# Optimization experiments

Measured on AMD Instinct MI355X. Metric: run time of the kernel, lower is better.

## Reference

```python
import jax, jax.numpy as jnp
import numpy as np

D_MODEL = 1024
N_HEADS = 16
D_Q = D_MODEL // N_HEADS
NEG = float(-2**32 + 1)


def setup_inputs() -> dict:
    key = jax.random.key(0)
    ks = jax.random.split(key, 8)
    B, L = 8, 1024
    q = jax.random.normal(ks[0], (B, L, D_MODEL), dtype=jnp.float32)
    k = jax.random.normal(ks[1], (B, L, D_MODEL), dtype=jnp.float32)
    # causal subsequent mask: 1 above the diagonal (positions to be masked)
    subseq_mask = jnp.broadcast_to(
        jnp.triu(jnp.ones((L, L), dtype=jnp.int32), k=1), (B, L, L))
    s = 1.0 / np.sqrt(D_MODEL)
    Wq = jax.random.normal(ks[2], (D_MODEL, D_MODEL), dtype=jnp.float32) * s
    Wk = jax.random.normal(ks[3], (D_MODEL, D_MODEL), dtype=jnp.float32) * s
    Wv = jax.random.normal(ks[4], (D_MODEL, D_MODEL), dtype=jnp.float32) * s
    bq = jax.random.normal(ks[5], (D_MODEL,), dtype=jnp.float32) * 0.01
    bk = jax.random.normal(ks[6], (D_MODEL,), dtype=jnp.float32) * 0.01
    bv = jax.random.normal(ks[7], (D_MODEL,), dtype=jnp.float32) * 0.01
    return {"q": q, "k": k, "subseq_mask": subseq_mask,
            "Wq": Wq, "bq": bq, "Wk": Wk, "bk": bk, "Wv": Wv, "bv": bv}


def reference(q, k, subseq_mask, Wq, bq, Wk, bk, Wv, bv):
    B, Lq, _ = q.shape
    Lk = k.shape[1]
    residual = q
    # projections; heads laid out as (H, B, L, d_q) matching torch permute(2,0,1,3)
    qp = (q @ Wq + bq).reshape(B, Lq, N_HEADS, D_Q).transpose(2, 0, 1, 3)
    kp = (k @ Wk + bk).reshape(B, Lk, N_HEADS, D_Q).transpose(2, 0, 1, 3)
    vp = (k @ Wv + bv).reshape(B, Lk, N_HEADS, D_Q).transpose(2, 0, 1, 3)
    # scaled scores: (H, B, Lq, Lk)
    scores = jnp.einsum('hbqd,hbkd->hbqk', qp, kp) / np.sqrt(D_Q)
    # key mask from PROJECTED k (faithful to source)
    key_masks = jnp.sign(jnp.abs(jnp.sum(kp, -1)))          # (H, B, Lk)
    scores = jnp.where(key_masks[:, :, None, :] == 0, NEG, scores)
    # subsequence (causal) mask, replicated over heads
    scores = jnp.where(subseq_mask[None, :, :, :] == 1, NEG, scores)
    attn = jax.nn.softmax(scores, axis=-1)
    # post-softmax query mask from PROJECTED q (faithful to source)
    query_masks = jnp.sign(jnp.abs(jnp.sum(qp, -1)))        # (H, B, Lq)
    attn = attn * query_masks[:, :, :, None]
    # dropout is identity in eval/reference mode
    out = jnp.einsum('hbqk,hbkd->hbqd', attn, vp)           # (H, B, Lq, d_q)
    out = out.transpose(1, 2, 0, 3).reshape(B, Lq, N_HEADS * D_Q)
    return out + residual
```

## Files before the change

kernel.cpp:

```cpp
#include <hip/hip_runtime.h>
#include <cstdint>
#include <cstddef>

#define DM 1024
#define NH 16
#define DQ 64
#define NB 8
#define LSEQ 1024

typedef __attribute__((ext_vector_type(8))) short short8;
typedef __attribute__((ext_vector_type(4))) float floatx4;

__device__ __forceinline__ unsigned short f2bf(float f) {
  union { float f; unsigned u; } v; v.f = f;
  unsigned r = v.u + 0x7FFFu + ((v.u >> 16) & 1u);
  return (unsigned short)(r >> 16);
}
__device__ __forceinline__ float bf2f(unsigned short u) {
  union { unsigned u; float f; } v; v.u = ((unsigned)u) << 16;
  return v.f;
}

__device__ __forceinline__ void async_load16(const void* g, void* l) {
  __builtin_amdgcn_global_load_lds(
      (const __attribute__((address_space(1))) unsigned int*)g,
      (__attribute__((address_space(3))) unsigned int*)l, 16, 0, 0);
}

__global__ void convert_qk(const float* __restrict__ q, const float* __restrict__ k,
                           unsigned short* __restrict__ qb, unsigned short* __restrict__ kb) {
  size_t i = ((size_t)blockIdx.x * 256 + threadIdx.x) * 4;
  float4 a = *(const float4*)&q[i];
  ushort4 r;
  r.x = f2bf(a.x); r.y = f2bf(a.y); r.z = f2bf(a.z); r.w = f2bf(a.w);
  *(ushort4*)&qb[i] = r;
  float4 b = *(const float4*)&k[i];
  ushort4 s;
  s.x = f2bf(b.x); s.y = f2bf(b.y); s.z = f2bf(b.z); s.w = f2bf(b.w);
  *(ushort4*)&kb[i] = s;
}

__global__ void transpose_w(const float* __restrict__ Wq, const float* __restrict__ Wk,
                            const float* __restrict__ Wv, unsigned short* __restrict__ Wt) {
  int z = blockIdx.z;
  const float* W = (z == 0) ? Wq : (z == 1) ? Wk : Wv;
  __shared__ float tile[32][33];
  int n0 = blockIdx.x * 32, k0 = blockIdx.y * 32;
  int tx = threadIdx.x;
  for (int j = threadIdx.y; j < 32; j += 8)
    tile[j][tx] = W[(size_t)(k0 + j) * DM + n0 + tx];
  __syncthreads();
  unsigned short* o = Wt + (size_t)z * DM * DM;
  for (int j = threadIdx.y; j < 32; j += 8)
    o[(size_t)(n0 + j) * DM + k0 + tx] = f2bf(tile[tx][j]);
}

__global__ __launch_bounds__(256) void gemm_proj(
    const unsigned short* __restrict__ qb, const unsigned short* __restrict__ kb,
    const unsigned short* __restrict__ Wt,
    const float* __restrict__ bq, const float* __restrict__ bk, const float* __restrict__ bv,
    unsigned short* __restrict__ Pq, unsigned short* __restrict__ Pk,
    unsigned short* __restrict__ Pvt,
    float* __restrict__ qmask, float* __restrict__ kmask) {
  const int z = blockIdx.z;
  const unsigned short* A = (z == 0) ? qb : kb;
  const unsigned short* Bt = Wt + (size_t)z * DM * DM;
  const float* bias = (z == 0) ? bq : (z == 1) ? bk : bv;

  __shared__ unsigned short smem[8704];
  unsigned short* As = smem;
  unsigned short* Bs = smem + 4096;

  const int tid = threadIdx.x;
  const int lane = tid & 63;
  const int wave = tid >> 6;
  const int l16 = lane & 15, quad = lane >> 4;
  const int wm = wave & 1, wn = wave >> 1;
  const int rowBase = blockIdx.y * 128;
  const int colBase = blockIdx.x * 128;

  floatx4 acc[4][4];
  const floatx4 zf = {0.f, 0.f, 0.f, 0.f};
#pragma unroll
  for (int i = 0; i < 4; i++)
#pragma unroll
    for (int j = 0; j < 4; j++) acc[i][j] = zf;

  for (int kt = 0; kt < DM; kt += 32) {
#pragma unroll
    for (int c = wave; c < 8; c += 4) {
      async_load16(A + (size_t)(rowBase + c * 16 + (lane >> 2)) * DM + kt + (lane & 3) * 8, &As[c * 512]);
      async_load16(Bt + (size_t)(colBase + c * 16 + (lane >> 2)) * DM + kt + (lane & 3) * 8, &Bs[c * 512]);
    }
    __syncthreads();

    short8 af[4], bfr[4];
#pragma unroll
    for (int i = 0; i < 4; i++)
      af[i] = *(const short8*)&As[(wm * 64 + i * 16 + l16) * 32 + quad * 8];
#pragma unroll
    for (int j = 0; j < 4; j++)
      bfr[j] = *(const short8*)&Bs[(wn * 64 + j * 16 + l16) * 32 + quad * 8];
#pragma unroll
    for (int i = 0; i < 4; i++)
#pragma unroll
      for (int j = 0; j < 4; j++)
        acc[i][j] = __builtin_amdgcn_mfma_f32_16x16x32_bf16(af[i], bfr[j], acc[i][j], 0, 0, 0);
    __syncthreads();
  }

#pragma unroll
  for (int j = 0; j < 4; j++) {
    const float bj = bias[colBase + wn * 64 + j * 16 + l16];
#pragma unroll
    for (int i = 0; i < 4; i++)
#pragma unroll
      for (int r = 0; r < 4; r++) acc[i][j][r] += bj;
  }

  if (z < 2) {
    float* mask = (z == 0) ? qmask : kmask;
    const int h = (colBase >> 6) + wn;
#pragma unroll
    for (int i = 0; i < 4; i++)
#pragma unroll
      for (int r = 0; r < 4; r++) {
        float rs = acc[i][0][r] + acc[i][1][r] + acc[i][2][r] + acc[i][3][r];
        rs += __shfl_xor(rs, 1);
        rs += __shfl_xor(rs, 2);
        rs += __shfl_xor(rs, 4);
        rs += __shfl_xor(rs, 8);
        if (l16 == 0) {
          const int row = rowBase + wm * 64 + i * 16 + quad * 4 + r;
          mask[((size_t)((row >> 10) * NH + h)) * LSEQ + (row & 1023)] = (rs != 0.f) ? 1.f : 0.f;
        }
      }
    unsigned short* P = (z == 0) ? Pq : Pk;
#pragma unroll
    for (int j = 0; j < 4; j++) {
      const int col = colBase + wn * 64 + j * 16 + l16;
      const int hh = col >> 6, d = col & 63;
#pragma unroll
      for (int i = 0; i < 4; i++) {
        const int row0 = rowBase + wm * 64 + i * 16 + quad * 4;
#pragma unroll
        for (int r = 0; r < 4; r++) {
          const int rr = row0 + r;
          P[((size_t)((rr >> 10) * NH + hh) * LSEQ + (rr & 1023)) * DQ + d] = f2bf(acc[i][j][r]);
        }
      }
    }
  } else {
    const int b = rowBase >> 10;
    const int l0r = rowBase & 1023;
#pragma unroll
    for (int j = 0; j < 4; j++) {
      __syncthreads();
#pragma unroll
      for (int i = 0; i < 4; i++) {
        ushort4 v;
        v.x = f2bf(acc[i][j][0]); v.y = f2bf(acc[i][j][1]);
        v.z = f2bf(acc[i][j][2]); v.w = f2bf(acc[i][j][3]);
        *(ushort4*)&smem[(wn * 16 + l16) * 136 + wm * 64 + i * 16 + quad * 4] = v;
      }
      __syncthreads();
      const int c = tid >> 3, seg = tid & 7;
      const int col = colBase + (c >> 4) * 64 + j * 16 + (c & 15);
      const int hh = col >> 6, d = col & 63;
      int4 t0 = *(const int4*)&smem[c * 136 + seg * 16];
      int4 t1 = *(const int4*)&smem[c * 136 + seg * 16 + 8];
      const size_t g = ((size_t)((b * NH + hh) * DQ + d)) * LSEQ + l0r + seg * 16;
      *(int4*)&Pvt[g] = t0;
      *(int4*)&Pvt[g + 8] = t1;
    }
  }
}

__global__ __launch_bounds__(256, 3) void attn_kernel(
    const unsigned short* __restrict__ Q, const unsigned short* __restrict__ K,
    const unsigned short* __restrict__ Vt,
    const float* __restrict__ kmask, const float* __restrict__ qmask,
    const float* __restrict__ qin, float* __restrict__ out) {
  const int bh = blockIdx.x;
  const int qblk = blockIdx.y;
  const int b = bh >> 4, h = bh & 15;
  const size_t base = (size_t)bh * LSEQ * DQ;

  const int tid = threadIdx.x;
  const int lane = tid & 63;
  const int wave = tid >> 6;
  const int l16 = lane & 15, quad = lane >> 4;
  const int qw = qblk * 128 + wave * 32;

  __shared__ unsigned short Ks[2 * 4096];
  __shared__ unsigned short Vs[2 * 4096];
  __shared__ unsigned short Ps[4][2304];

  short8 qf[2][2];
#pragma unroll
  for (int sub = 0; sub < 2; sub++)
#pragma unroll
    for (int c = 0; c < 2; c++) {
      short8 t = *(const short8*)&Q[base + (size_t)(qw + sub * 16 + l16) * DQ + c * 32 + quad * 8];
#pragma unroll
      for (int e = 0; e < 8; e++) t[e] = (short)f2bf(bf2f((unsigned short)t[e]) * 0.125f);
      qf[sub][c] = t;
    }

  const floatx4 zf = {0.f, 0.f, 0.f, 0.f};
  floatx4 o[2][4];
#pragma unroll
  for (int sub = 0; sub < 2; sub++)
#pragma unroll
    for (int jj = 0; jj < 4; jj++) o[sub][jj] = zf;
  float l_p[2][4] = {{0.f, 0.f, 0.f, 0.f}, {0.f, 0.f, 0.f, 0.f}};

  const int swz = (quad ^ (l16 & 7)) * 8;
  const int swz2 = ((quad + 4) ^ (l16 & 7)) * 8;
  const int vswz = (quad ^ (l16 >> 1)) * 8;
  const int vswz2 = ((quad + 4) ^ (l16 >> 1)) * 8;

  const int srl = (lane >> 3);
  const int ktiles = (qblk + 1) * 2;
  const int tmax = 2 * qblk + (wave >> 1);

  {
    const int kt0 = 0;
#pragma unroll
    for (int cc = wave; cc < 8; cc += 4) {
      const int rl = cc * 8 + srl;
      const int ck = ((lane & 7) ^ (rl & 7)) * 8;
      async_load16(&K[base + (size_t)(kt0 + rl) * DQ + ck], &Ks[cc * 512]);
      const int cv = ((lane & 7) ^ ((rl >> 1) & 7)) * 8;
      async_load16(&Vt[base + (size_t)rl * LSEQ + kt0 + cv], &Vs[cc * 512]);
    }
  }
  __syncthreads();

  for (int t = 0; t < ktiles; t++) {
    const int cur = t & 1;
    const int kt = t * 64;
    const bool live = (t <= tmax);

    float km[4];
    if (live) {
#pragma unroll
      for (int ct = 0; ct < 4; ct++) km[ct] = kmask[(size_t)bh * LSEQ + kt + ct * 16 + l16];
    }

    if (t + 1 < ktiles) {
      const int nkt = kt + 64;
      const int nb = (cur ^ 1) * 4096;
#pragma unroll
      for (int cc = wave; cc < 8; cc += 4) {
        const int rl = cc * 8 + srl;
        const int ck = ((lane & 7) ^ (rl & 7)) * 8;
        async_load16(&K[base + (size_t)(nkt + rl) * DQ + ck], &Ks[nb + cc * 512]);
        const int cv = ((lane & 7) ^ ((rl >> 1) & 7)) * 8;
        async_load16(&Vt[base + (size_t)rl * LSEQ + nkt + cv], &Vs[nb + cc * 512]);
      }
    }

    if (live) {
      const unsigned short* Kb = &Ks[cur * 4096];
      const unsigned short* Vb = &Vs[cur * 4096];
      const bool diag = (t == tmax);

#pragma unroll
      for (int sub = 0; sub < 2; sub++) {
        floatx4 s[4];
#pragma unroll
        for (int ct = 0; ct < 4; ct++) {
          const int kr = (ct * 16 + l16) * 64;
          const short8 kf0 = *(const short8*)&Kb[kr + swz];
          const short8 kf1 = *(const short8*)&Kb[kr + swz2];
          floatx4 sv = zf;
          sv = __builtin_amdgcn_mfma_f32_16x16x32_bf16(qf[sub][0], kf0, sv, 0, 0, 0);
          sv = __builtin_amdgcn_mfma_f32_16x16x32_bf16(qf[sub][1], kf1, sv, 0, 0, 0);
          s[ct] = sv;
        }
        const int row0 = qw + sub * 16 + quad * 4;
        unsigned short* pw = &Ps[wave][(sub * 16 + quad * 4) * 72];
        if (diag) {
#pragma unroll
          for (int ct = 0; ct < 4; ct++) {
            const int col = kt + ct * 16 + l16;
#pragma unroll
            for (int r = 0; r < 4; r++) {
              float e = __expf(s[ct][r]) * km[ct];
              e = (col <= row0 + r) ? e : 0.f;
              l_p[sub][r] += e;
              pw[r * 72 + ct * 16 + l16] = f2bf(e);
            }
          }
        } else {
#pragma unroll
          for (int ct = 0; ct < 4; ct++) {
#pragma unroll
            for (int r = 0; r < 4; r++) {
              float e = __expf(s[ct][r]) * km[ct];
              l_p[sub][r] += e;
              pw[r * 72 + ct * 16 + l16] = f2bf(e);
            }
          }
        }
      }
      asm volatile("s_waitcnt lgkmcnt(0)" ::: "memory");

      short8 pf[2][2];
#pragma unroll
      for (int sub = 0; sub < 2; sub++) {
        pf[sub][0] = *(const short8*)&Ps[wave][(sub * 16 + l16) * 72 + quad * 8];
        pf[sub][1] = *(const short8*)&Ps[wave][(sub * 16 + l16) * 72 + 32 + quad * 8];
      }
#pragma unroll
      for (int jj = 0; jj < 4; jj++) {
        const int vr = (jj * 16 + l16) * 64;
        const short8 vf0 = *(const short8*)&Vb[vr + vswz];
        const short8 vf1 = *(const short8*)&Vb[vr + vswz2];
#pragma unroll
        for (int sub = 0; sub < 2; sub++) {
          o[sub][jj] = __builtin_amdgcn_mfma_f32_16x16x32_bf16(pf[sub][0], vf0, o[sub][jj], 0, 0, 0);
          o[sub][jj] = __builtin_amdgcn_mfma_f32_16x16x32_bf16(pf[sub][1], vf1, o[sub][jj], 0, 0, 0);
        }
      }
    }
    __syncthreads();
  }

  const int hd = h * DQ;
#pragma unroll
  for (int sub = 0; sub < 2; sub++)
#pragma unroll
    for (int r = 0; r < 4; r++) {
      float lv = l_p[sub][r];
      lv += __shfl_xor(lv, 1);
      lv += __shfl_xor(lv, 2);
      lv += __shfl_xor(lv, 4);
      lv += __shfl_xor(lv, 8);
      const int row = qw + sub * 16 + quad * 4 + r;
      const float inv = qmask[(size_t)bh * LSEQ + row] / lv;
#pragma unroll
      for (int jj = 0; jj < 4; jj++) {
        const size_t oi = ((size_t)(b * LSEQ + row)) * DM + hd + jj * 16 + l16;
        out[oi] = o[sub][jj][r] * inv + qin[oi];
      }
    }
}

extern "C" void kernel_launch(void* const* d_in, const int* in_sizes, int n_in,
                              void* d_out, int out_size, void* d_ws, size_t ws_size,
                              hipStream_t stream) {
  const float* q = (const float*)d_in[0];
  const float* k = (const float*)d_in[1];
  const float* Wq = (const float*)d_in[3];
  const float* bq = (const float*)d_in[4];
  const float* Wk = (const float*)d_in[5];
  const float* bk = (const float*)d_in[6];
  const float* Wv = (const float*)d_in[7];
  const float* bv = (const float*)d_in[8];
  float* out = (float*)d_out;

  char* w = (char*)d_ws;
  unsigned short* qb = (unsigned short*)(w + 0);
  unsigned short* kb = (unsigned short*)(w + 16777216);
  unsigned short* Wt = (unsigned short*)(w + 33554432);
  unsigned short* Pq = (unsigned short*)(w + 39845888);
  unsigned short* Pk = (unsigned short*)(w + 56623104);
  unsigned short* Pvt = (unsigned short*)(w + 73400320);
  float* qmask = (float*)(w + 90177536);
  float* kmask = (float*)(w + 90701824);

  convert_qk<<<8192, 256, 0, stream>>>(q, k, qb, kb);
  transpose_w<<<dim3(32, 32, 3), dim3(32, 8), 0, stream>>>(Wq, Wk, Wv, Wt);
  gemm_proj<<<dim3(8, 64, 3), 256, 0, stream>>>(qb, kb, Wt, bq, bk, bv, Pq, Pk, Pvt, qmask, kmask);
  attn_kernel<<<dim3(128, 8), 256, 0, stream>>>(Pq, Pk, Pvt, kmask, qmask, q, out);
}
```

Measured before the change: 280.9 us.

## Deepen GEMM K-tile with swizzled LDS, reorder grids, schedule heavy attention blocks first

The projection GEMM now stages 64-wide K slices with an XOR-swizzled LDS layout, halving the number of barrier-separated iterations and avoiding bank conflicts. Its grid is transposed so consecutive blocks share the same weight columns. The attention kernel processes causal query blocks in reverse order so the longest blocks launch first, and both kernels request higher occupancy through launch bounds. An unused pointer parameter is added. Larger LDS use and tighter register limits could cause spills or reduce occupancy.

```diff
diff --git a/kernel.cpp b/kernel.cpp
--- a/kernel.cpp
+++ b/kernel.cpp
@@ -55,10 +55,11 @@
     o[(size_t)(n0 + j) * DM + k0 + tx] = f2bf(tile[tx][j]);
 }
 
-__global__ __launch_bounds__(256) void gemm_proj(
+__global__ __launch_bounds__(256, 4) void gemm_proj(
     const unsigned short* __restrict__ qb, const unsigned short* __restrict__ kb,
     const unsigned short* __restrict__ Wt,
     const float* __restrict__ bq, const float* __restrict__ bk, const float* __restrict__ bv,
+    const float* __restrict__ ,
     unsigned short* __restrict__ Pq, unsigned short* __restrict__ Pk,
     unsigned short* __restrict__ Pvt,
     float* __restrict__ qmask, float* __restrict__ kmask) {
@@ -67,17 +68,17 @@
   const unsigned short* Bt = Wt + (size_t)z * DM * DM;
   const float* bias = (z == 0) ? bq : (z == 1) ? bk : bv;
 
-  __shared__ unsigned short smem[8704];
+  __shared__ unsigned short smem[16384];
   unsigned short* As = smem;
-  unsigned short* Bs = smem + 4096;
+  unsigned short* Bs = smem + 8192;
 
   const int tid = threadIdx.x;
   const int lane = tid & 63;
   const int wave = tid >> 6;
   const int l16 = lane & 15, quad = lane >> 4;
   const int wm = wave & 1, wn = wave >> 1;
-  const int rowBase = blockIdx.y * 128;
-  const int colBase = blockIdx.x * 128;
+  const int rowBase = blockIdx.x * 128;
+  const int colBase = blockIdx.y * 128;
 
   floatx4 acc[4][4];
   const floatx4 zf = {0.f, 0.f, 0.f, 0.f};
@@ -86,26 +87,35 @@
 #pragma unroll
     for (int j = 0; j < 4; j++) acc[i][j] = zf;
 
-  for (int kt = 0; kt < DM; kt += 32) {
-#pragma unroll
-    for (int c = wave; c < 8; c += 4) {
-      async_load16(A + (size_t)(rowBase + c * 16 + (lane >> 2)) * DM + kt + (lane & 3) * 8, &As[c * 512]);
-      async_load16(Bt + (size_t)(colBase + c * 16 + (lane >> 2)) * DM + kt + (lane & 3) * 8, &Bs[c * 512]);
+  const int srl = lane >> 3;
+  const int sl7 = lane & 7;
+
+  for (int kt = 0; kt < DM; kt += 64) {
+#pragma unroll
+    for (int cc = wave; cc < 16; cc += 4) {
+      const int rl = cc * 8 + srl;
+      const int ck = (sl7 ^ (rl & 7)) * 8;
+      async_load16(A + (size_t)(rowBase + rl) * DM + kt + ck, &As[cc * 512]);
+      async_load16(Bt + (size_t)(colBase + rl) * DM + kt + ck, &Bs[cc * 512]);
     }
     __syncthreads();
 
-    short8 af[4], bfr[4];
-#pragma unroll
-    for (int i = 0; i < 4; i++)
-      af[i] = *(const short8*)&As[(wm * 64 + i * 16 + l16) * 32 + quad * 8];
-#pragma unroll
-    for (int j = 0; j < 4; j++)
-      bfr[j] = *(const short8*)&Bs[(wn * 64 + j * 16 + l16) * 32 + quad * 8];
-#pragma unroll
-    for (int i = 0; i < 4; i++)
+#pragma unroll
+    for (int c = 0; c < 2; c++) {
+      const int chnk = ((c << 2) + quad) ^ (l16 & 7);
+      short8 af[4], bfr[4];
+#pragma unroll
+      for (int i = 0; i < 4; i++)
+        af[i] = *(const short8*)&As[(wm * 64 + i * 16 + l16) * 64 + chnk * 8];
 #pragma unroll
       for (int j = 0; j < 4; j++)
-        acc[i][j] = __builtin_amdgcn_mfma_f32_16x16x32_bf16(af[i], bfr[j], acc[i][j], 0, 0, 0);
+        bfr[j] = *(const short8*)&Bs[(wn * 64 + j * 16 + l16) * 64 + chnk * 8];
+#pragma unroll
+      for (int i = 0; i < 4; i++)
+#pragma unroll
+        for (int j = 0; j < 4; j++)
+          acc[i][j] = __builtin_amdgcn_mfma_f32_16x16x32_bf16(af[i], bfr[j], acc[i][j], 0, 0, 0);
+    }
     __syncthreads();
   }
 
@@ -176,13 +186,13 @@
   }
 }
 
-__global__ __launch_bounds__(256, 3) void attn_kernel(
+__global__ __launch_bounds__(256, 4) void attn_kernel(
     const unsigned short* __restrict__ Q, const unsigned short* __restrict__ K,
     const unsigned short* __restrict__ Vt,
     const float* __restrict__ kmask, const float* __restrict__ qmask,
     const float* __restrict__ qin, float* __restrict__ out) {
   const int bh = blockIdx.x;
-  const int qblk = blockIdx.y;
+  const int qblk = 7 - blockIdx.y;
   const int b = bh >> 4, h = bh & 15;
   const size_t base = (size_t)bh * LSEQ * DQ;
 
@@ -225,14 +235,13 @@
   const int tmax = 2 * qblk + (wave >> 1);
 
   {
-    const int kt0 = 0;
 #pragma unroll
     for (int cc = wave; cc < 8; cc += 4) {
       const int rl = cc * 8 + srl;
       const int ck = ((lane & 7) ^ (rl & 7)) * 8;
-      async_load16(&K[base + (size_t)(kt0 + rl) * DQ + ck], &Ks[cc * 512]);
+      async_load16(&K[base + (size_t)rl * DQ + ck], &Ks[cc * 512]);
       const int cv = ((lane & 7) ^ ((rl >> 1) & 7)) * 8;
-      async_load16(&Vt[base + (size_t)rl * LSEQ + kt0 + cv], &Vs[cc * 512]);
+      async_load16(&Vt[base + (size_t)rl * LSEQ + cv], &Vs[cc * 512]);
     }
   }
   __syncthreads();
@@ -373,6 +382,7 @@
 
   convert_qk<<<8192, 256, 0, stream>>>(q, k, qb, kb);
   transpose_w<<<dim3(32, 32, 3), dim3(32, 8), 0, stream>>>(Wq, Wk, Wv, Wt);
-  gemm_proj<<<dim3(8, 64, 3), 256, 0, stream>>>(qb, kb, Wt, bq, bk, bv, Pq, Pk, Pvt, qmask, kmask);
+  gemm_proj<<<dim3(64, 8, 3), 256, 0, stream>>>(qb, kb, Wt, bq, bk, bv, nullptr,
+                                                Pq, Pk, Pvt, qmask, kmask);
   attn_kernel<<<dim3(128, 8), 256, 0, stream>>>(Pq, Pk, Pvt, kmask, qmask, q, out);
 }
```

Result: faster. 252.8 us (-10.0%).
